# Kernel tuning notes

Hardware: AMD Instinct MI355X
Metric: run time of the kernel (lower is better)

## Reference

```python
import jax, jax.numpy as jnp
import numpy as np

N_NODES = 50000
N_EDGES = 800000
HIDDEN = 128
NUM_LAYERS = 3
NEG_SLOPE = 0.2  # PyG GATConv default leaky_relu slope


def setup_inputs() -> dict:
    key = jax.random.key(0)
    ks = jax.random.split(key, 10)
    d = HIDDEN
    glorot = 1.0 / np.sqrt(d)
    inp = {
        "x": jax.random.normal(ks[0], (N_NODES, d), dtype=jnp.float32),
        "edge_index": jax.random.randint(ks[1], (2, N_EDGES), 0, N_NODES, dtype=jnp.int32),
        "edge_mask": jax.random.uniform(ks[2], (N_EDGES,), dtype=jnp.float32),
        # GATConv params (heads=1)
        "W_gat": jax.random.normal(ks[3], (d, d), dtype=jnp.float32) * glorot,
        "a_src": jax.random.normal(ks[4], (d,), dtype=jnp.float32) * glorot,
        "a_dst": jax.random.normal(ks[5], (d,), dtype=jnp.float32) * glorot,
        "b_gat": jnp.zeros((d,), dtype=jnp.float32),
        # Stacked GCNConv params
        "W_gcn": jax.random.normal(ks[6], (NUM_LAYERS, d, d), dtype=jnp.float32) * glorot,
        "b_gcn": jnp.zeros((NUM_LAYERS, d), dtype=jnp.float32),
    }
    return inp


def _seg_softmax(e, seg, n):
    m = jax.ops.segment_max(e, seg, num_segments=n)
    p = jnp.exp(e - m[seg])
    s = jax.ops.segment_sum(p, seg, num_segments=n)
    return p / s[seg]


def reference(x, edge_index, edge_mask, W_gat, a_src, a_dst, b_gat, W_gcn, b_gcn):
    N = x.shape[0]
    loops = jnp.arange(N, dtype=edge_index.dtype)
    src = jnp.concatenate([edge_index[0], loops])  # [E+N] with self loops
    dst = jnp.concatenate([edge_index[1], loops])

    # --- GATConv (heads=1, add_self_loops=True); edge_attr ignored (edge_dim=None) ---
    xp = x @ W_gat                                      # [N, d]
    e = jax.nn.leaky_relu((xp @ a_src)[src] + (xp @ a_dst)[dst], NEG_SLOPE)
    alpha = _seg_softmax(e, dst, N)                     # segment softmax over incoming edges
    h = jax.ops.segment_sum(alpha[:, None] * xp[src], dst, num_segments=N) + b_gat

    # --- GCN normalization with edge_mask as edge_weight (self-loop weight = 1) ---
    w = jnp.concatenate([edge_mask, jnp.ones((N,), dtype=edge_mask.dtype)])
    deg = jax.ops.segment_sum(w, dst, num_segments=N)
    dinv = jnp.where(deg > 0, jax.lax.rsqrt(jnp.maximum(deg, 1e-12)), 0.0)
    norm = dinv[src] * w * dinv[dst]                    # [E+N]

    outs = [h]
    for l in range(NUM_LAYERS):
        z = outs[-1] @ W_gcn[l]                         # [N, d]
        z = jax.ops.segment_sum(norm[:, None] * z[src], dst, num_segments=N) + b_gcn[l]
        outs.append(jax.nn.relu(z))

    # JumpingKnowledge 'max': elementwise max over layer outputs
    return jnp.max(jnp.stack(outs, axis=0), axis=0)
```

## Files before the change

### kernel.cpp

```cpp
#include <hip/hip_runtime.h>

#define HIDDEN 128
#define NEG_SLOPE 0.2f
#define P_SORT 256

typedef unsigned short ushort_t;
typedef __attribute__((ext_vector_type(8))) short short8;
typedef __attribute__((ext_vector_type(4))) float floatx4;

static inline size_t align_up(size_t x, size_t a){ return (x + a - 1) & ~(a - 1); }

__device__ __forceinline__ ushort_t f2b(float f){
  unsigned u = __float_as_uint(f);
  unsigned r = (u + 0x7FFFu + ((u >> 16) & 1u)) >> 16;
  return (ushort_t)r;
}

__device__ __forceinline__ float b2f(ushort_t u){
  return __uint_as_float(((unsigned)u) << 16);
}

__device__ __forceinline__ void fma8q(float* acc, uint2 v, float a){
  int x = (int)v.x, y = (int)v.y;
  acc[0] += a * (float)((x << 24) >> 24);
  acc[1] += a * (float)((x << 16) >> 24);
  acc[2] += a * (float)((x <<  8) >> 24);
  acc[3] += a * (float)( x        >> 24);
  acc[4] += a * (float)((y << 24) >> 24);
  acc[5] += a * (float)((y << 16) >> 24);
  acc[6] += a * (float)((y <<  8) >> 24);
  acc[7] += a * (float)( y        >> 24);
}

__device__ __forceinline__ uint2 packq8(const float* f, float qi){
  unsigned a = 0, b = 0;
  int q;
  q = (int)rintf(f[0]*qi); a |= ((unsigned)q & 255u);
  q = (int)rintf(f[1]*qi); a |= ((unsigned)q & 255u) << 8;
  q = (int)rintf(f[2]*qi); a |= ((unsigned)q & 255u) << 16;
  q = (int)rintf(f[3]*qi); a |= ((unsigned)q & 255u) << 24;
  q = (int)rintf(f[4]*qi); b |= ((unsigned)q & 255u);
  q = (int)rintf(f[5]*qi); b |= ((unsigned)q & 255u) << 8;
  q = (int)rintf(f[6]*qi); b |= ((unsigned)q & 255u) << 16;
  q = (int)rintf(f[7]*qi); b |= ((unsigned)q & 255u) << 24;
  uint2 r; r.x = a; r.y = b; return r;
}

__device__ __forceinline__ uint4 pack8(const float* f){
  uint4 u;
  u.x = (unsigned)f2b(f[0]) | ((unsigned)f2b(f[1]) << 16);
  u.y = (unsigned)f2b(f[2]) | ((unsigned)f2b(f[3]) << 16);
  u.z = (unsigned)f2b(f[4]) | ((unsigned)f2b(f[5]) << 16);
  u.w = (unsigned)f2b(f[6]) | ((unsigned)f2b(f[7]) << 16);
  return u;
}


__global__ __launch_bounds__(256) void k_b1cnt_cast(const int* __restrict__ dst,
                                                    int* __restrict__ bcnt,
                                                    const float* __restrict__ Wg,
                                                    const float* __restrict__ Wc,
                                                    ushort_t* __restrict__ Wt,
                                                    int E, int epb, int nbkt){
  int t = threadIdx.x;
  if (blockIdx.x >= P_SORT){
    int i = (blockIdx.x - P_SORT)*256 + t;
    int mat = i >> 14, idx = i & 16383;
    int k = idx >> 7, n = idx & 127;
    float v = (mat == 0) ? Wg[idx] : Wc[(mat-1)*16384 + idx];
    Wt[mat*16384 + n*128 + k] = f2b(v);
    return;
  }
  __shared__ unsigned c[256];
  c[t] = 0;
  __syncthreads();
  int e0 = blockIdx.x * epb;
  int e1 = min(E, e0 + epb);
  for (int e = e0 + t; e < e1; e += 256) atomicAdd(&c[dst[e] >> 8], 1u);
  __syncthreads();
  if (t < nbkt) bcnt[t * P_SORT + blockIdx.x] = (int)c[t];
}

__global__ void k_scan1(const int* __restrict__ in, int* __restrict__ incl,
                        int* __restrict__ blockSums, int M){
  __shared__ int sd[256];
  int t = threadIdx.x;
  int i = blockIdx.x*256 + t;
  int v = (i < M) ? in[i] : 0;
  sd[t] = v; __syncthreads();
  for (int off = 1; off < 256; off <<= 1){
    int add = (t >= off) ? sd[t-off] : 0;
    __syncthreads();
    sd[t] += add;
    __syncthreads();
  }
  if (i < M) incl[i] = sd[t];
  if (t == 255) blockSums[blockIdx.x] = sd[255];
}

__global__ void k_scan2(const int* __restrict__ blockSums, int* __restrict__ blockOffs, int nb){
  __shared__ int sd[256];
  __shared__ int carry;
  int t = threadIdx.x;
  if (t == 0) carry = 0;
  __syncthreads();
  for (int base = 0; base < nb; base += 256){
    int i = base + t;
    int v = (i < nb) ? blockSums[i] : 0;
    sd[t] = v; __syncthreads();
    for (int off = 1; off < 256; off <<= 1){
      int add = (t >= off) ? sd[t-off] : 0;
      __syncthreads();
      sd[t] += add;
      __syncthreads();
    }
    if (i < nb) blockOffs[i] = carry + sd[t] - v;
    __syncthreads();
    if (t == 0) carry += sd[255];
    __syncthreads();
  }
}

__global__ __launch_bounds__(256) void k_b1place(const int* __restrict__ src,
                                                 const int* __restrict__ dst,
                                                 const float* __restrict__ w,
                                                 const int* __restrict__ incl,
                                                 const int* __restrict__ bcnt,
                                                 const int* __restrict__ blockOffs,
                                                 int2* __restrict__ tpw,
                                                 int E, int epb, int nbkt){
  __shared__ int base_[256];
  __shared__ unsigned c[256];
  int t = threadIdx.x;
  c[t] = 0;
  if (t < nbkt){
    int idx = t * P_SORT + blockIdx.x;
    base_[t] = incl[idx] - bcnt[idx] + blockOffs[t];
  }
  __syncthreads();
  int e0 = blockIdx.x * epb;
  int e1 = min(E, e0 + epb);
  for (int e = e0 + t; e < e1; e += 256){
    int d = dst[e];
    int b = d >> 8;
    unsigned r = atomicAdd(&c[b], 1u);
    int pos = base_[b] + (int)r;
    tpw[pos] = make_int2((int)((unsigned)src[e] | ((unsigned)(d & 255) << 16)),
                         __float_as_int(w[e]));
  }
}

__global__ __launch_bounds__(256) void k_b2(const int2* __restrict__ tpw,
                                            const int* __restrict__ blockOffs,
                                            int2* __restrict__ col_sw,
                                            int* __restrict__ rowp,
                                            float* __restrict__ dinv,
                                            int N, int E, int nbkt){
  __shared__ int cnt[4096];
  __shared__ int tsum[256];
  __shared__ float wsum[256];
  int b = blockIdx.x, t = threadIdx.x;
  int e0 = blockOffs[b];
  int e1 = (b + 1 < nbkt) ? blockOffs[b + 1] : E;
  #pragma unroll
  for (int i = 0; i < 16; i++) cnt[t*16 + i] = 0;
  wsum[t] = 0.f;
  __syncthreads();
  for (int e = e0 + t; e < e1; e += 256){
    int2 pw = tpw[e];
    unsigned dl = ((unsigned)pw.x >> 16) & 255u;
    unsigned s  = ((unsigned)pw.x & 0xFFFFu) >> 12;
    atomicAdd(&cnt[(dl << 4) | s], 1);
  }
  __syncthreads();
  int loc[16]; int run = 0;
  #pragma unroll
  for (int i = 0; i < 16; i++){ loc[i] = run; run += cnt[t*16 + i]; }
  tsum[t] = run;
  __syncthreads();
  for (int off = 1; off < 256; off <<= 1){
    int add = (t >= off) ? tsum[t-off] : 0;
    __syncthreads();
    tsum[t] += add;
    __syncthreads();
  }
  int base = tsum[t] - run;
  #pragma unroll
  for (int i = 0; i < 16; i++) cnt[t*16 + i] = base + loc[i];
  int node = b*256 + t;
  if (node < N) rowp[node] = e0 + base;
  if (b == 0 && t == 0) rowp[N] = E;
  __syncthreads();
  for (int e = e0 + t; e < e1; e += 256){
    int2 pw = tpw[e];
    unsigned dl = ((unsigned)pw.x >> 16) & 255u;
    unsigned srcv = (unsigned)pw.x & 0xFFFFu;
    unsigned s = srcv >> 12;
    int pos = e0 + atomicAdd(&cnt[(dl << 4) | s], 1);
    col_sw[pos] = make_int2((int)srcv, pw.y);
    atomicAdd(&wsum[dl], __int_as_float(pw.y));
  }
  __syncthreads();
  if (node < N) dinv[node] = rsqrtf(wsum[t] + 1.0f);
}

__global__ __launch_bounds__(128) void k_gemm1(const float* __restrict__ Ain,
                                               const ushort_t* __restrict__ Wt,
                                               unsigned* __restrict__ zq,
                                               float* __restrict__ sc_z,
                                               const float* __restrict__ a_src,
                                               const float* __restrict__ a_dst,
                                               const float* __restrict__ dinv,
                                               float2* __restrict__ attr,
                                               float* __restrict__ sdst, int M){
  __shared__ uint4 zq8v[64][8];
  char (*zq8)[128] = (char(*)[128])zq8v;
  int wave = threadIdx.x >> 6, l = threadIdx.x & 63;
  int q = l >> 4, lm = l & 15;
  int rowBase = blockIdx.x*64 + wave*32;
  floatx4 acc[2][8];
  #pragma unroll
  for (int mt = 0; mt < 2; mt++)
    #pragma unroll
    for (int nt = 0; nt < 8; nt++) acc[mt][nt] = (floatx4){0.f,0.f,0.f,0.f};

  #pragma unroll
  for (int kc = 0; kc < 4; kc++){
    int k0 = kc*32 + q*8;
    short8 a[2];
    #pragma unroll
    for (int mt = 0; mt < 2; mt++){
      long r = rowBase + mt*16 + lm;
      if (r < M){
        const float* ap = Ain + r*128 + k0;
        float4 u = *(const float4*)ap;
        float4 v = *(const float4*)(ap + 4);
        short8 tv;
        tv[0]=(short)f2b(u.x); tv[1]=(short)f2b(u.y); tv[2]=(short)f2b(u.z); tv[3]=(short)f2b(u.w);
        tv[4]=(short)f2b(v.x); tv[5]=(short)f2b(v.y); tv[6]=(short)f2b(v.z); tv[7]=(short)f2b(v.w);
        a[mt] = tv;
      } else a[mt] = (short8){0,0,0,0,0,0,0,0};
    }
    #pragma unroll
    for (int nt = 0; nt < 8; nt++){
      short8 b = *(const short8*)(Wt + (nt*16 + lm)*128 + k0);
      acc[0][nt] = __builtin_amdgcn_mfma_f32_16x16x32_bf16(a[0], b, acc[0][nt], 0, 0, 0);
      acc[1][nt] = __builtin_amdgcn_mfma_f32_16x16x32_bf16(a[1], b, acc[1][nt], 0, 0, 0);
    }
  }
  #pragma unroll
  for (int mt = 0; mt < 2; mt++){
    #pragma unroll
    for (int r = 0; r < 4; r++){
      float rm = 0.f;
      #pragma unroll
      for (int nt = 0; nt < 8; nt++) rm = fmaxf(rm, fabsf(acc[mt][nt][r]));
      #pragma unroll
      for (int off = 1; off <= 8; off <<= 1) rm = fmaxf(rm, __shfl_xor(rm, off, 64));
      float qi = (rm > 0.f) ? 127.f/rm : 0.f;
      int lrow = wave*32 + mt*16 + q*4 + r;
      #pragma unroll
      for (int nt = 0; nt < 8; nt++)
        zq8[lrow][nt*16 + lm] = (char)(int)rintf(acc[mt][nt][r]*qi);
      long row = rowBase + mt*16 + q*4 + r;
      if (lm == 0 && row < M) sc_z[row] = rm * (1.f/127.f);
    }
  }
  float as8[8], ad8[8];
  #pragma unroll
  for (int nt = 0; nt < 8; nt++){ as8[nt] = a_src[nt*16 + lm]; ad8[nt] = a_dst[nt*16 + lm]; }
  #pragma unroll
  for (int mt = 0; mt < 2; mt++){
    #pragma unroll
    for (int r = 0; r < 4; r++){
      float ps = 0.f, pd = 0.f;
      #pragma unroll
      for (int nt = 0; nt < 8; nt++){
        ps += acc[mt][nt][r] * as8[nt];
        pd += acc[mt][nt][r] * ad8[nt];
      }
      #pragma unroll
      for (int off = 1; off <= 8; off <<= 1){
        ps += __shfl_xor(ps, off, 64);
        pd += __shfl_xor(pd, off, 64);
      }
      long row = rowBase + mt*16 + q*4 + r;
      if (lm == 0 && row < M){
        attr[row] = make_float2(ps, dinv[row]);
        sdst[row] = pd;
      }
    }
  }
  __syncthreads();
  {
    int t = threadIdx.x;
    int lrow = t >> 1, half = t & 1;
    long row = (long)blockIdx.x*64 + lrow;
    if (row < M){
      uint4* dq = (uint4*)zq + row*8 + half*4;
      #pragma unroll
      for (int k = 0; k < 4; k++) dq[k] = zq8v[lrow][half*4 + k];
    }
  }
}

__global__ __launch_bounds__(256) void k_agg0(const unsigned* __restrict__ zq,
                                              const float* __restrict__ sc_z,
                                              const int* __restrict__ rowp,
                                              const int2* __restrict__ col_sw,
                                              int2* __restrict__ col_ea,
                                              const float2* __restrict__ attr,
                                              const float* __restrict__ sdst_,
                                              const float* __restrict__ bias,
                                              ushort_t* __restrict__ out,
                                              unsigned* __restrict__ g0,
                                              float* __restrict__ scd0, int N){
  int n = blockIdx.x*4 + (threadIdx.x >> 6);
  if (n >= N) return;
  int l = threadIdx.x & 63;
  int rs = rowp[n], re = rowp[n+1];
  float2 an = attr[n];
  float sdd = sdst_[n];
  float es = an.x + sdd;
  es = (es >= 0.f) ? es : NEG_SLOPE*es;
  float pself = __expf(es);
  float ps = 0.f;
  for (int j = rs + l; j < re; j += 64){
    int2 sw = col_sw[j];
    float2 a = attr[sw.x];
    float ee = a.x + sdd;
    ee = (ee >= 0.f) ? ee : NEG_SLOPE*ee;
    float pe = __expf(ee);
    ps += pe;
    col_ea[j] = make_int2(sw.x, __float_as_int(pe * sc_z[sw.x]));
  }
  #pragma unroll
  for (int off = 32; off >= 1; off >>= 1) ps += __shfl_xor(ps, off, 64);
  float inv = 1.f / (ps + pself);

  int sub = l >> 4, q = l & 15;
  const uint2* f8 = (const uint2*)zq;
  float acc[8] = {0.f,0.f,0.f,0.f,0.f,0.f,0.f,0.f};
  for (int base = rs; base < re; base += 24){
    int2 p[6]; float a[6];
    #pragma unroll
    for (int j = 0; j < 6; j++){
      int e = base + sub + 4*j;
      int cc = min(e, re-1);
      p[j] = col_ea[cc];
      a[j] = (e < re) ? __int_as_float(p[j].y) : 0.f;
    }
    uint2 v[6];
    #pragma unroll
    for (int j = 0; j < 6; j++) v[j] = f8[(size_t)p[j].x*16 + q];
    #pragma unroll
    for (int j = 0; j < 6; j++) fma8q(acc, v[j], a[j]);
  }
  #pragma unroll
  for (int j = 0; j < 8; j++){
    acc[j] += __shfl_xor(acc[j], 16, 64);
    acc[j] += __shfl_xor(acc[j], 32, 64);
  }
  if (sub == 0){
    #pragma unroll
    for (int j = 0; j < 8; j++) acc[j] *= inv;
    fma8q(acc, f8[(size_t)n*16 + q], pself * inv * sc_z[n]);
    float4 b0 = ((const float4*)bias)[q*2];
    float4 b1 = ((const float4*)bias)[q*2 + 1];
    acc[0]+=b0.x; acc[1]+=b0.y; acc[2]+=b0.z; acc[3]+=b0.w;
    acc[4]+=b1.x; acc[5]+=b1.y; acc[6]+=b1.z; acc[7]+=b1.w;
    ((uint4*)out)[(size_t)n*16 + q] = pack8(acc);
    float rm = 0.f;
    #pragma unroll
    for (int j = 0; j < 8; j++) rm = fmaxf(rm, fabsf(acc[j]));
    #pragma unroll
    for (int off = 1; off <= 8; off <<= 1) rm = fmaxf(rm, __shfl_xor(rm, off, 64));
    float qi = (rm > 0.f) ? 127.f/rm : 0.f;
    ((uint2*)g0)[(size_t)n*16 + q] = packq8(acc, qi);
    if (l == 0) scd0[n] = rm * (1.f/127.f) * an.y;
  }
}

__global__ __launch_bounds__(256) void k_ecoef(const int2* __restrict__ col_sw,
                                               const float* __restrict__ scd,
                                               int2* __restrict__ col_eq, int E){
  int e = blockIdx.x*256 + threadIdx.x;
  if (e < E){
    int2 sw = col_sw[e];
    col_eq[e] = make_int2(sw.x, __float_as_int(__int_as_float(sw.y) * scd[sw.x]));
  }
}

template<int MODE>
__global__ __launch_bounds__(256) void k_fagg(const unsigned* __restrict__ gin,
                                              const float* __restrict__ scd_prev,
                                              const int* __restrict__ rowp,
                                              const int2* __restrict__ col_eq,
                                              const float* __restrict__ dinv,
                                              const ushort_t* __restrict__ Wl,
                                              const float* __restrict__ bias,
                                              ushort_t* __restrict__ out,
                                              unsigned* __restrict__ gout,
                                              float* __restrict__ scd_out,
                                              const ushort_t* __restrict__ j0,
                                              const ushort_t* __restrict__ j1,
                                              const ushort_t* __restrict__ j2,
                                              float* __restrict__ yout, int N){
  __shared__ ushort_t At[16][136];
  __shared__ uint4 q8v[16][8];
  __shared__ unsigned rmaxs[16];
  char (*q8s)[128] = (char(*)[128])q8v;
  int wave = threadIdx.x >> 6, l = threadIdx.x & 63;
  int sub = l >> 4, q = l & 15;
  const uint2* f8 = (const uint2*)gin;
  int tile = blockIdx.x * 16;

  for (int i = 0; i < 4; i++){
    int row = wave*4 + i;
    int n = tile + row;
    int rs = 0, re = 0; float dn = 0.f, sprev = 0.f;
    if (n < N){ rs = rowp[n]; re = rowp[n+1]; dn = dinv[n]; sprev = scd_prev[n]; }
    float acc[8] = {0.f,0.f,0.f,0.f,0.f,0.f,0.f,0.f};
    for (int base = rs; base < re; base += 24){
      int2 p[6]; float a[6];
      #pragma unroll
      for (int j = 0; j < 6; j++){
        int e = base + sub + 4*j;
        int cc = min(e, re-1);
        p[j] = col_eq[cc];
        a[j] = (e < re) ? __int_as_float(p[j].y) : 0.f;
      }
      uint2 v[6];
      #pragma unroll
      for (int j = 0; j < 6; j++) v[j] = f8[(size_t)p[j].x*16 + q];
      #pragma unroll
      for (int j = 0; j < 6; j++) fma8q(acc, v[j], a[j]);
    }
    #pragma unroll
    for (int j = 0; j < 8; j++){
      acc[j] += __shfl_xor(acc[j], 16, 64);
      acc[j] += __shfl_xor(acc[j], 32, 64);
    }
    if (sub == 0){
      if (n < N) fma8q(acc, f8[(size_t)n*16 + q], sprev);
      #pragma unroll
      for (int j = 0; j < 8; j++) acc[j] *= dn;
      *(uint4*)&At[row][q*8] = pack8(acc);
    }
  }
  if (threadIdx.x < 16) rmaxs[threadIdx.x] = 0u;
  __syncthreads();

  floatx4 co[2];
  co[0] = (floatx4){0.f,0.f,0.f,0.f};
  co[1] = (floatx4){0.f,0.f,0.f,0.f};
  #pragma unroll
  for (int kc = 0; kc < 4; kc++){
    int k0 = kc*32 + sub*8;
    short8 a = *(const short8*)&At[q][k0];
    #pragma unroll
    for (int ntl = 0; ntl < 2; ntl++){
      int nt = wave*2 + ntl;
      short8 b = *(const short8*)(Wl + (size_t)(nt*16 + q)*128 + k0);
      co[ntl] = __builtin_amdgcn_mfma_f32_16x16x32_bf16(a, b, co[ntl], 0, 0, 0);
    }
  }
  float vv[4][2];
  #pragma unroll
  for (int r = 0; r < 4; r++){
    int row = sub*4 + r;
    int node = tile + row;
    float lmax = 0.f;
    #pragma unroll
    for (int ntl = 0; ntl < 2; ntl++){
      int colg = wave*32 + ntl*16 + q;
      float v = co[ntl][r] + bias[colg];
      v = fmaxf(v, 0.f);
      vv[r][ntl] = v;
      lmax = fmaxf(lmax, v);
      if (node < N){
        size_t idx = (size_t)node*128 + colg;
        if (MODE == 1){
          out[idx] = f2b(v);
        } else {
          float m = fmaxf(fmaxf(b2f(j0[idx]), b2f(j1[idx])),
                          fmaxf(b2f(j2[idx]), v));
          yout[idx] = m;
        }
      }
    }
    if (MODE == 1) atomicMax(&rmaxs[row], __float_as_uint(lmax));
  }
  if (MODE == 1){
    __syncthreads();
    #pragma unroll
    for (int r = 0; r < 4; r++){
      int row = sub*4 + r;
      float rm = __uint_as_float(rmaxs[row]);
      float qi = (rm > 0.f) ? 127.f/rm : 0.f;
      #pragma unroll
      for (int ntl = 0; ntl < 2; ntl++){
        int colg = wave*32 + ntl*16 + q;
        q8s[row][colg] = (char)(int)rintf(vv[r][ntl]*qi);
      }
    }
    if (threadIdx.x < 16){
      int node = tile + threadIdx.x;
      if (node < N){
        float rm = __uint_as_float(rmaxs[threadIdx.x]);
        scd_out[node] = rm * (1.f/127.f) * dinv[node];
      }
    }
    __syncthreads();
    if (threadIdx.x < 128){
      int row = threadIdx.x >> 3, c = threadIdx.x & 7;
      int node = tile + row;
      if (node < N) ((uint4*)gout)[(size_t)node*8 + c] = q8v[row][c];
    }
  }
}

extern "C" void kernel_launch(void* const* d_in, const int* in_sizes, int n_in,
                              void* d_out, int out_size, void* d_ws, size_t ws_size,
                              hipStream_t stream){
  const float* x      = (const float*)d_in[0];
  const int*   eidx   = (const int*)d_in[1];
  const float* emask  = (const float*)d_in[2];
  const float* W_gat  = (const float*)d_in[3];
  const float* a_src  = (const float*)d_in[4];
  const float* a_dst  = (const float*)d_in[5];
  const float* b_gat  = (const float*)d_in[6];
  const float* W_gcn  = (const float*)d_in[7];
  const float* b_gcn  = (const float*)d_in[8];
  int N = in_sizes[0] / HIDDEN;
  int E = in_sizes[1] / 2;
  const int* src = eidx;
  const int* dst = eidx + E;

  char* p = (char*)d_ws;
  auto carve = [&](size_t bytes)->char*{ char* q = p; p += align_up(bytes, 512); return q; };
  ushort_t* h0   = (ushort_t*)carve((size_t)N*HIDDEN*2);
  ushort_t* h1   = (ushort_t*)carve((size_t)N*HIDDEN*2);
  ushort_t* h2   = (ushort_t*)carve((size_t)N*HIDDEN*2);
  ushort_t* Wt   = (ushort_t*)carve((size_t)4*HIDDEN*HIDDEN*2);
  unsigned* zq   = (unsigned*)carve((size_t)N*HIDDEN);
  unsigned* g0q  = (unsigned*)carve((size_t)N*HIDDEN);
  unsigned* g1q  = (unsigned*)carve((size_t)N*HIDDEN);
  unsigned* g2q  = (unsigned*)carve((size_t)N*HIDDEN);
  float* sc_z    = (float*)carve((size_t)N*4);
  float* scd0    = (float*)carve((size_t)N*4);
  float* scd1    = (float*)carve((size_t)N*4);
  float* scd2    = (float*)carve((size_t)N*4);
  float2* attr   = (float2*)carve((size_t)N*8);
  float* sdst    = (float*)carve((size_t)N*4);
  float* dinv    = (float*)carve((size_t)N*4);
  int*   rowp    = (int*)  carve((size_t)(N+1)*4);
  int2*  col_sw  = (int2*) carve((size_t)E*8);
  int2*  col_ea  = (int2*) carve((size_t)E*8);
  int2*  tpw     = (int2*) carve((size_t)E*8);
  int nbkt = (N + 255) >> 8;
  int M    = nbkt * P_SORT;
  int*   bcnt  = (int*)carve((size_t)M*4);
  int*   incl  = (int*)carve((size_t)M*4);
  int nbs = (M + 255) / 256;
  int*   blockSums = (int*)carve((size_t)nbs*4);
  int*   blockOffs = (int*)carve((size_t)nbs*4);
  (void)ws_size; (void)n_in; (void)out_size;

  int epb = (E + P_SORT - 1) / P_SORT;
  int gb  = (N + 63) / 64;
  int nwb = (N + 3) / 4;
  int nfb = (N + 15) / 16;
  int neb = (E + 255) / 256;

  k_b1cnt_cast<<<P_SORT + 256, 256, 0, stream>>>(dst, bcnt, W_gat, W_gcn, Wt, E, epb, nbkt);
  k_scan1  <<<nbs, 256, 0, stream>>>(bcnt, incl, blockSums, M);
  k_scan2  <<<1,   256, 0, stream>>>(blockSums, blockOffs, nbs);
  k_b1place<<<P_SORT, 256, 0, stream>>>(src, dst, emask, incl, bcnt, blockOffs,
                                        tpw, E, epb, nbkt);
  k_b2     <<<nbkt, 256, 0, stream>>>(tpw, blockOffs, col_sw, rowp, dinv, N, E, nbkt);

  k_gemm1<<<gb, 128, 0, stream>>>(x, Wt, zq, sc_z, a_src, a_dst, dinv, attr, sdst, N);

  k_agg0<<<nwb, 256, 0, stream>>>(zq, sc_z, rowp, col_sw, col_ea, attr, sdst,
                                  b_gat, h0, g0q, scd0, N);

  k_ecoef<<<neb, 256, 0, stream>>>(col_sw, scd0, col_ea, E);
  k_fagg<1><<<nfb, 256, 0, stream>>>(g0q, scd0, rowp, col_ea, dinv,
                                     Wt + (size_t)1*16384, b_gcn + 0,
                                     h1, g1q, scd1,
                                     nullptr, nullptr, nullptr, nullptr, N);
  k_ecoef<<<neb, 256, 0, stream>>>(col_sw, scd1, col_ea, E);
  k_fagg<1><<<nfb, 256, 0, stream>>>(g1q, scd1, rowp, col_ea, dinv,
                                     Wt + (size_t)2*16384, b_gcn + 128,
                                     h2, g2q, scd2,
                                     nullptr, nullptr, nullptr, nullptr, N);
  k_ecoef<<<neb, 256, 0, stream>>>(col_sw, scd2, col_ea, E);
  k_fagg<2><<<nfb, 256, 0, stream>>>(g2q, scd2, rowp, col_ea, dinv,
                                     Wt + (size_t)3*16384, b_gcn + 256,
                                     nullptr, nullptr, nullptr,
                                     h0, h1, h2, (float*)d_out, N);
}
```

Baseline: 346.6 us.

## Fuse GAT edge-softmax pass into aggregation and interleave two rows in GCN aggregation

k_agg0 no longer makes a separate pass over edges to compute attention weights and write col_ea. It now computes exp scores inline while gathering features, and normalizes by the accumulated sum at the end. Per-node attention source score, dinv and the quantization scale are packed into one float4 so a single gather fetches all of them. In k_fagg each wave now processes two destination rows at once, with interleaved loads to expose more memory-level parallelism. The cost is more registers and a wider per-edge attr gather, plus wasted iterations when the two rows have unequal degree.

```diff
diff --git a/kernel.cpp b/kernel.cpp
--- a/kernel.cpp
+++ b/kernel.cpp
@@ -207,11 +207,10 @@
 __global__ __launch_bounds__(128) void k_gemm1(const float* __restrict__ Ain,
                                                const ushort_t* __restrict__ Wt,
                                                unsigned* __restrict__ zq,
-                                               float* __restrict__ sc_z,
                                                const float* __restrict__ a_src,
                                                const float* __restrict__ a_dst,
                                                const float* __restrict__ dinv,
-                                               float2* __restrict__ attr,
+                                               float4* __restrict__ attr4,
                                                float* __restrict__ sdst, int M){
   __shared__ uint4 zq8v[64][8];
   char (*zq8)[128] = (char(*)[128])zq8v;
@@ -248,6 +247,7 @@
       acc[1][nt] = __builtin_amdgcn_mfma_f32_16x16x32_bf16(a[1], b, acc[1][nt], 0, 0, 0);
     }
   }
+  float rms[2][4];
   #pragma unroll
   for (int mt = 0; mt < 2; mt++){
     #pragma unroll
@@ -262,8 +262,7 @@
       #pragma unroll
       for (int nt = 0; nt < 8; nt++)
         zq8[lrow][nt*16 + lm] = (char)(int)rintf(acc[mt][nt][r]*qi);
-      long row = rowBase + mt*16 + q*4 + r;
-      if (lm == 0 && row < M) sc_z[row] = rm * (1.f/127.f);
+      rms[mt][r] = rm * (1.f/127.f);
     }
   }
   float as8[8], ad8[8];
@@ -286,7 +285,7 @@
       }
       long row = rowBase + mt*16 + q*4 + r;
       if (lm == 0 && row < M){
-        attr[row] = make_float2(ps, dinv[row]);
+        attr4[row] = make_float4(ps, dinv[row], rms[mt][r], 0.f);
         sdst[row] = pd;
       }
     }
@@ -305,11 +304,9 @@
 }
 
 __global__ __launch_bounds__(256) void k_agg0(const unsigned* __restrict__ zq,
-                                              const float* __restrict__ sc_z,
                                               const int* __restrict__ rowp,
                                               const int2* __restrict__ col_sw,
-                                              int2* __restrict__ col_ea,
-                                              const float2* __restrict__ attr,
+                                              const float4* __restrict__ attr4,
                                               const float* __restrict__ sdst_,
                                               const float* __restrict__ bias,
                                               ushort_t* __restrict__ out,
@@ -318,44 +315,44 @@
   int n = blockIdx.x*4 + (threadIdx.x >> 6);
   if (n >= N) return;
   int l = threadIdx.x & 63;
+  int sub = l >> 4, q = l & 15;
   int rs = rowp[n], re = rowp[n+1];
-  float2 an = attr[n];
+  float4 an = attr4[n];
   float sdd = sdst_[n];
   float es = an.x + sdd;
   es = (es >= 0.f) ? es : NEG_SLOPE*es;
   float pself = __expf(es);
-  float ps = 0.f;
-  for (int j = rs + l; j < re; j += 64){
-    int2 sw = col_sw[j];
-    float2 a = attr[sw.x];
-    float ee = a.x + sdd;
-    ee = (ee >= 0.f) ? ee : NEG_SLOPE*ee;
-    float pe = __expf(ee);
-    ps += pe;
-    col_ea[j] = make_int2(sw.x, __float_as_int(pe * sc_z[sw.x]));
-  }
-  #pragma unroll
-  for (int off = 32; off >= 1; off >>= 1) ps += __shfl_xor(ps, off, 64);
-  float inv = 1.f / (ps + pself);
-
-  int sub = l >> 4, q = l & 15;
+
   const uint2* f8 = (const uint2*)zq;
   float acc[8] = {0.f,0.f,0.f,0.f,0.f,0.f,0.f,0.f};
+  float ps = 0.f;
+  int last = (re > rs) ? re - 1 : 0;
   for (int base = rs; base < re; base += 24){
-    int2 p[6]; float a[6];
+    int2 p[6];
     #pragma unroll
     for (int j = 0; j < 6; j++){
       int e = base + sub + 4*j;
-      int cc = min(e, re-1);
-      p[j] = col_ea[cc];
-      a[j] = (e < re) ? __int_as_float(p[j].y) : 0.f;
-    }
+      p[j] = col_sw[min(e, last)];
+    }
+    float4 at[6];
+    #pragma unroll
+    for (int j = 0; j < 6; j++) at[j] = attr4[p[j].x];
     uint2 v[6];
     #pragma unroll
     for (int j = 0; j < 6; j++) v[j] = f8[(size_t)p[j].x*16 + q];
     #pragma unroll
-    for (int j = 0; j < 6; j++) fma8q(acc, v[j], a[j]);
-  }
+    for (int j = 0; j < 6; j++){
+      int e = base + sub + 4*j;
+      float ee = at[j].x + sdd;
+      ee = (ee >= 0.f) ? ee : NEG_SLOPE*ee;
+      float pe = (e < re) ? __expf(ee) : 0.f;
+      ps += pe;
+      fma8q(acc, v[j], pe * at[j].z);
+    }
+  }
+  ps += __shfl_xor(ps, 16, 64);
+  ps += __shfl_xor(ps, 32, 64);
+  float inv = 1.f / (ps + pself);
   #pragma unroll
   for (int j = 0; j < 8; j++){
     acc[j] += __shfl_xor(acc[j], 16, 64);
@@ -364,7 +361,7 @@
   if (sub == 0){
     #pragma unroll
     for (int j = 0; j < 8; j++) acc[j] *= inv;
-    fma8q(acc, f8[(size_t)n*16 + q], pself * inv * sc_z[n]);
+    fma8q(acc, f8[(size_t)n*16 + q], pself * inv * an.z);
     float4 b0 = ((const float4*)bias)[q*2];
     float4 b1 = ((const float4*)bias)[q*2 + 1];
     acc[0]+=b0.x; acc[1]+=b0.y; acc[2]+=b0.z; acc[3]+=b0.w;
@@ -415,37 +412,64 @@
   const uint2* f8 = (const uint2*)gin;
   int tile = blockIdx.x * 16;
 
-  for (int i = 0; i < 4; i++){
-    int row = wave*4 + i;
-    int n = tile + row;
-    int rs = 0, re = 0; float dn = 0.f, sprev = 0.f;
-    if (n < N){ rs = rowp[n]; re = rowp[n+1]; dn = dinv[n]; sprev = scd_prev[n]; }
-    float acc[8] = {0.f,0.f,0.f,0.f,0.f,0.f,0.f,0.f};
-    for (int base = rs; base < re; base += 24){
-      int2 p[6]; float a[6];
+  #pragma unroll
+  for (int pair = 0; pair < 2; pair++){
+    int rowA = wave*4 + pair*2, rowB = rowA + 1;
+    int nA = tile + rowA, nB = tile + rowB;
+    int rsA = 0, reA = 0, rsB = 0, reB = 0;
+    float dnA = 0.f, spA = 0.f, dnB = 0.f, spB = 0.f;
+    if (nA < N){ rsA = rowp[nA]; reA = rowp[nA+1]; dnA = dinv[nA]; spA = scd_prev[nA]; }
+    if (nB < N){ rsB = rowp[nB]; reB = rowp[nB+1]; dnB = dinv[nB]; spB = scd_prev[nB]; }
+    int lastA = (reA > rsA) ? reA - 1 : 0;
+    int lastB = (reB > rsB) ? reB - 1 : 0;
+    float accA[8] = {0.f,0.f,0.f,0.f,0.f,0.f,0.f,0.f};
+    float accB[8] = {0.f,0.f,0.f,0.f,0.f,0.f,0.f,0.f};
+    int baseA = rsA, baseB = rsB;
+    while (baseA < reA || baseB < reB){
+      int2 pA[6], pB[6];
       #pragma unroll
       for (int j = 0; j < 6; j++){
-        int e = base + sub + 4*j;
-        int cc = min(e, re-1);
-        p[j] = col_eq[cc];
-        a[j] = (e < re) ? __int_as_float(p[j].y) : 0.f;
-      }
-      uint2 v[6];
-      #pragma unroll
-      for (int j = 0; j < 6; j++) v[j] = f8[(size_t)p[j].x*16 + q];
-      #pragma unroll
-      for (int j = 0; j < 6; j++) fma8q(acc, v[j], a[j]);
+        int e = baseA + sub + 4*j;
+        pA[j] = col_eq[min(e, lastA)];
+      }
+      #pragma unroll
+      for (int j = 0; j < 6; j++){
+        int e = baseB + sub + 4*j;
+        pB[j] = col_eq[min(e, lastB)];
+      }
+      uint2 vA[6], vB[6];
+      #pragma unroll
+      for (int j = 0; j < 6; j++) vA[j] = f8[(size_t)pA[j].x*16 + q];
+      #pragma unroll
+      for (int j = 0; j < 6; j++) vB[j] = f8[(size_t)pB[j].x*16 + q];
+      #pragma unroll
+      for (int j = 0; j < 6; j++){
+        int e = baseA + sub + 4*j;
+        fma8q(accA, vA[j], (e < reA) ? __int_as_float(pA[j].y) : 0.f);
+      }
+      #pragma unroll
+      for (int j = 0; j < 6; j++){
+        int e = baseB + sub + 4*j;
+        fma8q(accB, vB[j], (e < reB) ? __int_as_float(pB[j].y) : 0.f);
+      }
+      baseA += 24; baseB += 24;
     }
     #pragma unroll
     for (int j = 0; j < 8; j++){
-      acc[j] += __shfl_xor(acc[j], 16, 64);
-      acc[j] += __shfl_xor(acc[j], 32, 64);
+      accA[j] += __shfl_xor(accA[j], 16, 64);
+      accA[j] += __shfl_xor(accA[j], 32, 64);
+      accB[j] += __shfl_xor(accB[j], 16, 64);
+      accB[j] += __shfl_xor(accB[j], 32, 64);
     }
     if (sub == 0){
-      if (n < N) fma8q(acc, f8[(size_t)n*16 + q], sprev);
-      #pragma unroll
-      for (int j = 0; j < 8; j++) acc[j] *= dn;
-      *(uint4*)&At[row][q*8] = pack8(acc);
+      if (nA < N) fma8q(accA, f8[(size_t)nA*16 + q], spA);
+      #pragma unroll
+      for (int j = 0; j < 8; j++) accA[j] *= dnA;
+      *(uint4*)&At[rowA][q*8] = pack8(accA);
+      if (nB < N) fma8q(accB, f8[(size_t)nB*16 + q], spB);
+      #pragma unroll
+      for (int j = 0; j < 8; j++) accB[j] *= dnB;
+      *(uint4*)&At[rowB][q*8] = pack8(accB);
     }
   }
   if (threadIdx.x < 16) rmaxs[threadIdx.x] = 0u;
@@ -547,16 +571,15 @@
   unsigned* g0q  = (unsigned*)carve((size_t)N*HIDDEN);
   unsigned* g1q  = (unsigned*)carve((size_t)N*HIDDEN);
   unsigned* g2q  = (unsigned*)carve((size_t)N*HIDDEN);
-  float* sc_z    = (float*)carve((size_t)N*4);
   float* scd0    = (float*)carve((size_t)N*4);
   float* scd1    = (float*)carve((size_t)N*4);
   float* scd2    = (float*)carve((size_t)N*4);
-  float2* attr   = (float2*)carve((size_t)N*8);
+  float4* attr4  = (float4*)carve((size_t)N*16);
   float* sdst    = (float*)carve((size_t)N*4);
   float* dinv    = (float*)carve((size_t)N*4);
   int*   rowp    = (int*)  carve((size_t)(N+1)*4);
   int2*  col_sw  = (int2*) carve((size_t)E*8);
-  int2*  col_ea  = (int2*) carve((size_t)E*8);
+  int2*  col_eq  = (int2*) carve((size_t)E*8);
   int2*  tpw     = (int2*) carve((size_t)E*8);
   int nbkt = (N + 255) >> 8;
   int M    = nbkt * P_SORT;
@@ -580,23 +603,23 @@
                                         tpw, E, epb, nbkt);
   k_b2     <<<nbkt, 256, 0, stream>>>(tpw, blockOffs, col_sw, rowp, dinv, N, E, nbkt);
 
-  k_gemm1<<<gb, 128, 0, stream>>>(x, Wt, zq, sc_z, a_src, a_dst, dinv, attr, sdst, N);
-
-  k_agg0<<<nwb, 256, 0, stream>>>(zq, sc_z, rowp, col_sw, col_ea, attr, sdst,
+  k_gemm1<<<gb, 128, 0, stream>>>(x, Wt, zq, a_src, a_dst, dinv, attr4, sdst, N);
+
+  k_agg0<<<nwb, 256, 0, stream>>>(zq, rowp, col_sw, attr4, sdst,
                                   b_gat, h0, g0q, scd0, N);
 
-  k_ecoef<<<neb, 256, 0, stream>>>(col_sw, scd0, col_ea, E);
-  k_fagg<1><<<nfb, 256, 0, stream>>>(g0q, scd0, rowp, col_ea, dinv,
+  k_ecoef<<<neb, 256, 0, stream>>>(col_sw, scd0, col_eq, E);
+  k_fagg<1><<<nfb, 256, 0, stream>>>(g0q, scd0, rowp, col_eq, dinv,
                                      Wt + (size_t)1*16384, b_gcn + 0,
                                      h1, g1q, scd1,
                                      nullptr, nullptr, nullptr, nullptr, N);
-  k_ecoef<<<neb, 256, 0, stream>>>(col_sw, scd1, col_ea, E);
-  k_fagg<1><<<nfb, 256, 0, stream>>>(g1q, scd1, rowp, col_ea, dinv,
+  k_ecoef<<<neb, 256, 0, stream>>>(col_sw, scd1, col_eq, E);
+  k_fagg<1><<<nfb, 256, 0, stream>>>(g1q, scd1, rowp, col_eq, dinv,
                                      Wt + (size_t)2*16384, b_gcn + 128,
                                      h2, g2q, scd2,
                                      nullptr, nullptr, nullptr, nullptr, N);
-  k_ecoef<<<neb, 256, 0, stream>>>(col_sw, scd2, col_ea, E);
-  k_fagg<2><<<nfb, 256, 0, stream>>>(g2q, scd2, rowp, col_ea, dinv,
+  k_ecoef<<<neb, 256, 0, stream>>>(col_sw, scd2, col_eq, E);
+  k_fagg<2><<<nfb, 256, 0, stream>>>(g2q, scd2, rowp, col_eq, dinv,
                                      Wt + (size_t)3*16384, b_gcn + 256,
                                      nullptr, nullptr, nullptr,
                                      h0, h1, h2, (float*)d_out, N);
```

After: 345.0 us. Within noise of the previous version (-0.4%).
